# Kernel tuning notes

Hardware: AMD Instinct MI355X
Metric: run time of the kernel (lower is better)

The kernel has to match this reference:

```python
import jax, jax.numpy as jnp
import numpy as np
from jax import lax

B, N = 8, 107136          # batch, anchors (248*216*2)
SCORE_THRESH = 0.05
PRE_MAX = 2048            # nms_pre_max_sizes[0]
POST_MAX = 128            # nms_post_max_sizes[0]
IOU_THRESH = 0.5
NUM_DIR_BINS = 2
DIR_OFFSET = 0.0
POST_CENTER_RANGE = np.array([0.0, -39.68, -5.0, 69.12, 39.68, 5.0], np.float32)


def setup_inputs() -> dict:
    key = jax.random.key(0)
    k1, k2, k3, k4, k5 = jax.random.split(key, 5)
    box_preds = jax.random.normal(k1, (B, N, 7), jnp.float32) * 0.3
    cls_preds = jax.random.normal(k2, (B, N, 2), jnp.float32) * 2.0
    dir_preds = jax.random.normal(k3, (B, N, 2), jnp.float32)
    # realistic KITTI car anchors: (x, y, z, w, l, h, r)
    xs = jax.random.uniform(k4, (B, N), jnp.float32, 0.0, 69.12)
    ys = jax.random.uniform(k5, (B, N), jnp.float32, -39.68, 39.68)
    zs = jnp.full((B, N), -1.0, jnp.float32)
    w = jnp.full((B, N), 1.6, jnp.float32)
    l = jnp.full((B, N), 3.9, jnp.float32)
    h = jnp.full((B, N), 1.56, jnp.float32)
    r = jnp.broadcast_to(jnp.where(jnp.arange(N) % 2 == 0, 0.0, np.pi / 2).astype(jnp.float32), (B, N))
    anchors = jnp.stack([xs, ys, zs, w, l, h, r], axis=-1)
    return {"box_preds": box_preds, "cls_preds": cls_preds, "dir_preds": dir_preds, "anchors": anchors}


def _decode(bp, an):
    # GroundBox3dCoder.decode_torch (second/pointpillars), code order (x,y,z,w,l,h,r)
    xa, ya, za, wa, la, ha, ra = [an[..., i] for i in range(7)]
    xt, yt, zt, wt, lt, ht, rt = [bp[..., i] for i in range(7)]
    za = za + ha * 0.5
    diag = jnp.sqrt(la * la + wa * wa)
    xg = xt * diag + xa
    yg = yt * diag + ya
    zg = zt * ha + za
    lg = jnp.exp(lt) * la
    wg = jnp.exp(wt) * wa
    hg = jnp.exp(ht) * ha
    rg = rt + ra
    zg = zg - hg * 0.5
    return jnp.stack([xg, yg, zg, wg, lg, hg, rg], axis=-1)


def _standup(boxes):
    # boxes: [K,7] decoded; rotated 2d rect -> axis-aligned standup box (x1,y1,x2,y2)
    x, y, w, l, r = boxes[:, 0], boxes[:, 1], boxes[:, 3], boxes[:, 4], boxes[:, 6]
    c, s = jnp.abs(jnp.cos(r)), jnp.abs(jnp.sin(r))
    hx = 0.5 * (w * c + l * s)
    hy = 0.5 * (w * s + l * c)
    return jnp.stack([x - hx, y - hy, x + hx, y + hy], axis=-1)


def _pairwise_iou(bb):
    # bb: [K,4] standup boxes
    x1, y1, x2, y2 = bb[:, 0], bb[:, 1], bb[:, 2], bb[:, 3]
    area = (x2 - x1) * (y2 - y1)
    ix = jnp.maximum(0.0, jnp.minimum(x2[:, None], x2[None, :]) - jnp.maximum(x1[:, None], x1[None, :]))
    iy = jnp.maximum(0.0, jnp.minimum(y2[:, None], y2[None, :]) - jnp.maximum(y1[:, None], y1[None, :]))
    inter = ix * iy
    return inter / jnp.maximum(area[:, None] + area[None, :] - inter, 1e-8)


def _greedy_nms(ious, valid):
    K = valid.shape[0]
    idxs = jnp.arange(K)
    def body(i, keep):
        sup = (ious[i] > IOU_THRESH) & (idxs > i) & keep[i]
        return keep & ~sup
    return lax.fori_loop(0, K, body, valid)


def _limit_period(val, offset, period):
    return val - jnp.floor(val / period + offset) * period


def _predict_one(boxes, scores, dir_labels):
    # boxes [N,7], scores [N], dir_labels [N] int32 (already sorted? no: raw)
    masked = jnp.where(scores >= SCORE_THRESH, scores, -jnp.inf)
    top_s, idx = lax.top_k(masked, PRE_MAX)           # sorted desc
    b = boxes[idx]                                    # [K,7]
    dl = dir_labels[idx]
    valid = jnp.isfinite(top_s)
    ious = _pairwise_iou(_standup(b))
    keep = _greedy_nms(lax.stop_gradient(ious), valid)
    kept = jnp.where(keep, top_s, -jnp.inf)
    sel_s, sel_i = lax.top_k(kept, POST_MAX)
    sel_b = b[sel_i]
    sel_dl = dl[sel_i].astype(sel_b.dtype)
    period = 2.0 * np.pi / NUM_DIR_BINS
    dir_rot = _limit_period(sel_b[:, 6] - DIR_OFFSET, 0.0, period)
    new_r = dir_rot + DIR_OFFSET + period * sel_dl
    sel_b = jnp.concatenate([sel_b[:, :6], new_r[:, None]], axis=-1)
    pcr = jnp.asarray(POST_CENTER_RANGE)
    in_range = jnp.all(sel_b[:, :3] >= pcr[:3], axis=1) & jnp.all(sel_b[:, :3] <= pcr[3:], axis=1)
    mask = jnp.isfinite(sel_s) & in_range
    out_s = jnp.where(mask, sel_s, 0.0)
    out_b = jnp.where(mask[:, None], sel_b, 0.0)
    labels = jnp.zeros((POST_MAX,), jnp.int32)  # single fg class -> label 0
    return out_b, out_s, labels, mask


def reference(box_preds, cls_preds, dir_preds, anchors):
    decoded = _decode(box_preds, anchors)                    # [B,N,7]
    scores = jax.nn.softmax(cls_preds, axis=-1)[..., 1]      # [B,N]
    dir_labels = jnp.argmax(dir_preds, axis=-1).astype(jnp.int32)
    return jax.vmap(_predict_one)(decoded, scores, dir_labels)
```

## Files before the change

kernel.cpp:

```cpp
#include <hip/hip_runtime.h>
#include <stdint.h>

#define NB 8
#define NN 107136
#define TOTAL (NB * NN)
#define NPAIR (NN / 2)
#define PRE 2048
#define POST 128
#define CAP 4096
#define HBINS 128
#define KEYBASE 0xBF00u
#define SCORE_TH 0.05f
#define SH_BPB 53

static constexpr size_t OFF_SCORES = 0;
static constexpr size_t SZ_SCORES  = (size_t)TOTAL * 4;
static constexpr size_t OFF_HIST   = OFF_SCORES + SZ_SCORES;
static constexpr size_t SZ_HIST    = (size_t)NB * SH_BPB * HBINS * 4;
static constexpr size_t OFF_CNT    = OFF_HIST + SZ_HIST;
static constexpr size_t SZ_CNT     = (size_t)NB * 64 * 4;
static constexpr size_t OFF_CAND   = OFF_CNT + SZ_CNT + 256;
static constexpr size_t SZ_CAND    = (size_t)NB * CAP * 8;
static constexpr size_t OFF_SELS   = OFF_CAND + SZ_CAND;
static constexpr size_t OFF_SELI   = OFF_SELS + (size_t)NB * PRE * 4;
static constexpr size_t OFF_SELB   = OFF_SELI + (size_t)NB * PRE * 4;
static constexpr size_t OFF_SBB    = OFF_SELB + (size_t)NB * PRE * 7 * 4;
static constexpr size_t OFF_SAR    = OFF_SBB + (size_t)NB * PRE * 4 * 4;
static constexpr size_t OFF_MASK   = OFF_SAR + (size_t)NB * PRE * 4;
static constexpr size_t SZ_MASK    = (size_t)NB * PRE * 32 * 8;


__global__ void __launch_bounds__(256) k_scoreshist(const float* __restrict__ cls,
                                                    float* __restrict__ scores,
                                                    uint32_t* __restrict__ hp,
                                                    uint32_t* __restrict__ counts,
                                                    uint64_t* __restrict__ cand) {
    int b = blockIdx.y;
    int t = threadIdx.x;
    if (blockIdx.x == 0 && t == 0) counts[(size_t)b * 64] = 0u;
    if (blockIdx.x < 16)
        cand[(size_t)b * CAP + blockIdx.x * 256 + t] = 0ull;
    __shared__ uint32_t lh[HBINS];
    if (t < HBINS) lh[t] = 0u;
    __syncthreads();
    const float4* cp = (const float4*)cls + (size_t)b * NPAIR;
    float2* sp = (float2*)scores + (size_t)b * NPAIR;
#pragma unroll
    for (int k = 0; k < 4; k++) {
        int p = blockIdx.x * 1024 + k * 256 + t;
        if (p < NPAIR) {
            float4 c = cp[p];
            float m0 = fmaxf(c.x, c.y);
            float s0 = __fdiv_rn(expf(__fsub_rn(c.y, m0)),
                                 __fadd_rn(expf(__fsub_rn(c.x, m0)), expf(__fsub_rn(c.y, m0))));
            float m1 = fmaxf(c.z, c.w);
            float s1 = __fdiv_rn(expf(__fsub_rn(c.w, m1)),
                                 __fadd_rn(expf(__fsub_rn(c.z, m1)), expf(__fsub_rn(c.w, m1))));
            sp[p] = make_float2(s0, s1);
            if (s0 >= 0.5f) {
                uint32_t bin = ((__float_as_uint(s0) >> 16) | 0x8000u) - KEYBASE;
                if (bin > 127u) bin = 127u;
                atomicAdd(&lh[bin], 1u);
            }
            if (s1 >= 0.5f) {
                uint32_t bin = ((__float_as_uint(s1) >> 16) | 0x8000u) - KEYBASE;
                if (bin > 127u) bin = 127u;
                atomicAdd(&lh[bin], 1u);
            }
        }
    }
    __syncthreads();
    if (t < HBINS) hp[((size_t)b * SH_BPB + blockIdx.x) * HBINS + t] = lh[t];
}

__global__ void __launch_bounds__(256) k_compact(const float* __restrict__ scores,
                                                 const uint32_t* __restrict__ hp,
                                                 uint32_t* __restrict__ counts,
                                                 uint64_t* __restrict__ cand) {
    int g2 = blockIdx.x * 256 + threadIdx.x;
    int lane = threadIdx.x & 63, wid = threadIdx.x >> 6;
    int e0 = 2 * g2;
    int b = e0 / NN;

    uint32_t h0 = 0, h1 = 0;
    const uint32_t* hb = hp + (size_t)b * SH_BPB * HBINS;
#pragma unroll 4
    for (int sg = 0; sg < SH_BPB; sg++) {
        h0 += hb[sg * HBINS + 2 * lane];
        h1 += hb[sg * HBINS + 2 * lane + 1];
    }
    uint32_t v = h0 + h1;
    for (int off = 1; off < 64; off <<= 1) {
        uint32_t u = __shfl_down(v, off);
        if (lane + off >= 64) u = 0u;
        v += u;
    }
    uint32_t total = __shfl(v, 0);
    int c = -1;
    if (v - h0 >= PRE) c = 2 * lane + 1;
    else if (v >= PRE) c = 2 * lane;
    for (int off = 32; off > 0; off >>= 1) c = max(c, __shfl_xor(c, off));
    uint32_t Tb = (total >= PRE && c >= 0) ? (KEYBASE + (uint32_t)c) : 0u;

    float2 sv = ((const float2*)scores)[g2];
    uint32_t key0 = __float_as_uint(sv.x) | 0x80000000u;
    uint32_t key1 = __float_as_uint(sv.y) | 0x80000000u;
    bool p0 = (sv.x >= SCORE_TH) && ((key0 >> 16) >= Tb);
    bool p1 = (sv.y >= SCORE_TH) && ((key1 >> 16) >= Tb);
    uint64_t bal0 = __ballot(p0), bal1 = __ballot(p1);
    uint32_t n0 = (uint32_t)__popcll(bal0);
    uint32_t wcnt = n0 + (uint32_t)__popcll(bal1);
    uint64_t below = (1ull << lane) - 1ull;
    uint32_t off0 = (uint32_t)__popcll(bal0 & below);
    uint32_t off1 = n0 + (uint32_t)__popcll(bal1 & below);
    __shared__ uint32_t lcnt[2];
    __shared__ uint32_t gbase[2];
    __shared__ uint32_t wbase[4];
    int b0 = (blockIdx.x * 512) / NN;
    if (threadIdx.x < 2) lcnt[threadIdx.x] = 0u;
    __syncthreads();
    if (lane == 0 && wcnt) wbase[wid] = atomicAdd(&lcnt[b - b0], wcnt);
    __syncthreads();
    if (threadIdx.x < 2 && lcnt[threadIdx.x])
        gbase[threadIdx.x] = atomicAdd(&counts[(size_t)(b0 + threadIdx.x) * 64], lcnt[threadIdx.x]);
    __syncthreads();
    if (p0 | p1) {
        uint32_t base = gbase[b - b0] + wbase[wid];
        if (p0) {
            uint32_t slot = base + off0;
            if (slot < CAP)
                cand[(size_t)b * CAP + slot] =
                    ((uint64_t)key0 << 32) | (uint64_t)(0xFFFFFFFFu - (uint32_t)(e0 - b * NN));
        }
        if (p1) {
            uint32_t slot = base + off1;
            if (slot < CAP)
                cand[(size_t)b * CAP + slot] =
                    ((uint64_t)key1 << 32) | (uint64_t)(0xFFFFFFFFu - (uint32_t)(e0 + 1 - b * NN));
        }
    }
}

__global__ void __launch_bounds__(256) k_rank_decode(
        const uint64_t* __restrict__ cand, const uint32_t* __restrict__ counts,
        const float* __restrict__ box_preds, const float* __restrict__ anchors,
        float* __restrict__ selS, uint32_t* __restrict__ selI,
        float* __restrict__ selB, float* __restrict__ selBB, float* __restrict__ selA) {
    int b = blockIdx.y;
    int m = (int)counts[(size_t)b * 64]; if (m > CAP) m = CAP;
    int i0 = blockIdx.x * 256;
    if (i0 >= m) return;
    int t = threadIdx.x;
    int i = i0 + t;
    const uint64_t* cb = cand + (size_t)b * CAP;
    uint64_t mykey = (i < m) ? cb[i] : ~0ull;
    __shared__ uint64_t tile[512];
    uint32_t rank = 0;
    int ntiles = (m + 511) >> 9;
    for (int tt = 0; tt < ntiles; tt++) {
        int base = tt << 9;
        tile[t] = cb[base + t];
        tile[t + 256] = cb[base + 256 + t];
        __syncthreads();
#pragma unroll 16
        for (int j = 0; j < 512; j++)
            rank += (tile[j] > mykey) ? 1u : 0u;
        __syncthreads();
    }
    if (i >= m || rank >= PRE) return;

    size_t o = (size_t)b * PRE + rank;
    uint32_t key = (uint32_t)(mykey >> 32);
    uint32_t idx = 0xFFFFFFFFu - (uint32_t)(mykey & 0xFFFFFFFFull);
    float score = __uint_as_float(key & 0x7FFFFFFFu);
    const float* bp = box_preds + ((size_t)b * NN + idx) * 7;
    const float* an = anchors + ((size_t)b * NN + idx) * 7;
    float xa = an[0], ya = an[1], za = an[2], wa = an[3], la = an[4], ha = an[5], ra = an[6];
    float xt = bp[0], yt = bp[1], zt = bp[2], wt = bp[3], lt = bp[4], ht = bp[5], rt = bp[6];
    float za2  = __fadd_rn(za, __fmul_rn(ha, 0.5f));
    float diag = sqrtf(__fadd_rn(__fmul_rn(la, la), __fmul_rn(wa, wa)));
    float xg = __fadd_rn(__fmul_rn(xt, diag), xa);
    float yg = __fadd_rn(__fmul_rn(yt, diag), ya);
    float zg = __fadd_rn(__fmul_rn(zt, ha), za2);
    float lg = __fmul_rn(expf(lt), la);
    float wg = __fmul_rn(expf(wt), wa);
    float hg = __fmul_rn(expf(ht), ha);
    float rg = __fadd_rn(rt, ra);
    zg = __fsub_rn(zg, __fmul_rn(hg, 0.5f));
    selS[o] = score; selI[o] = idx;
    selB[o * 7 + 0] = xg; selB[o * 7 + 1] = yg; selB[o * 7 + 2] = zg;
    selB[o * 7 + 3] = wg; selB[o * 7 + 4] = lg; selB[o * 7 + 5] = hg;
    selB[o * 7 + 6] = rg;
    float cc = fabsf(cosf(rg)), ss = fabsf(sinf(rg));
    float hx = __fmul_rn(0.5f, __fadd_rn(__fmul_rn(wg, cc), __fmul_rn(lg, ss)));
    float hy = __fmul_rn(0.5f, __fadd_rn(__fmul_rn(wg, ss), __fmul_rn(lg, cc)));
    float x1 = __fsub_rn(xg, hx), y1 = __fsub_rn(yg, hy);
    float x2 = __fadd_rn(xg, hx), y2 = __fadd_rn(yg, hy);
    selBB[o * 4 + 0] = x1; selBB[o * 4 + 1] = y1;
    selBB[o * 4 + 2] = x2; selBB[o * 4 + 3] = y2;
    selA[o] = __fmul_rn(__fsub_rn(x2, x1), __fsub_rn(y2, y1));
}

__global__ void __launch_bounds__(256) k_iou(const float* __restrict__ selBB,
                                             const float* __restrict__ selA,
                                             uint64_t* __restrict__ maskrows) {
    int b = blockIdx.y;
    int r0 = blockIdx.x * 32;
    __shared__ float sx1[PRE], sy1[PRE], sx2[PRE], sy2[PRE], sar[PRE];
    int t = threadIdx.x;
    for (int i = t; i < PRE; i += 256) {
        const float* p = selBB + ((size_t)b * PRE + i) * 4;
        sx1[i] = p[0]; sy1[i] = p[1]; sx2[i] = p[2]; sy2[i] = p[3];
        sar[i] = selA[(size_t)b * PRE + i];
    }
    __syncthreads();
    int w  = t & 31;
    int rl = t >> 5;
    int jbase = w * 64;
    float rx1[4], ry1[4], rx2[4], ry2[4], rar[4];
    int rows[4];
#pragma unroll
    for (int p = 0; p < 4; p++) {
        int i = r0 + rl * 4 + p;
        rows[p] = i;
        rx1[p] = sx1[i]; ry1[p] = sy1[i]; rx2[p] = sx2[i]; ry2[p] = sy2[i]; rar[p] = sar[i];
    }
    uint64_t bits[4] = {0, 0, 0, 0};
    for (int jj = 0; jj < 64; jj++) {
        int j = jbase + ((jj + w) & 63);
        float xj1 = sx1[j], yj1 = sy1[j], xj2 = sx2[j], yj2 = sy2[j], aj = sar[j];
#pragma unroll
        for (int p = 0; p < 4; p++) {
            float ix = fmaxf(0.f, __fsub_rn(fminf(rx2[p], xj2), fmaxf(rx1[p], xj1)));
            float iy = fmaxf(0.f, __fsub_rn(fminf(ry2[p], yj2), fmaxf(ry1[p], yj1)));
            float inter = __fmul_rn(ix, iy);
            float den = fmaxf(__fsub_rn(__fadd_rn(rar[p], aj), inter), 1e-8f);
            if (inter > __fmul_rn(0.5f, den) && j > rows[p])
                bits[p] |= (1ull << (j - jbase));
        }
    }
#pragma unroll
    for (int p = 0; p < 4; p++)
        maskrows[((size_t)b * PRE + rows[p]) * 32 + w] = bits[p];
}

__global__ void __launch_bounds__(128) k_nms_final(
        const uint64_t* __restrict__ maskrows, const float* __restrict__ selS,
        const uint32_t* __restrict__ selI, const float* __restrict__ selB,
        const uint32_t* __restrict__ counts, const float* __restrict__ dir_preds,
        float* __restrict__ out) {
    int b = blockIdx.x;
    __shared__ int keptIdx[POST];
    __shared__ int keptCount;
    int t = threadIdx.x;
    int Mv = (int)counts[(size_t)b * 64]; if (Mv > PRE) Mv = PRE;
    if (t < 64) {
        uint64_t removed = 0ull;
        int kc = 0;
        const uint64_t* mb = maskrows + (size_t)b * PRE * 32;
        uint64_t pre[8];
#pragma unroll
        for (int d = 0; d < 8; d++)
            pre[d] = (t < 32 && d < Mv) ? mb[(size_t)d * 32 + t] : 0ull;
        for (int i = 0; i < Mv && kc < POST; i++) {
            uint64_t mrow = pre[i & 7];
            int nf = i + 8;
            pre[i & 7] = (t < 32 && nf < Mv) ? mb[(size_t)nf * 32 + t] : 0ull;
            uint64_t rw = __shfl(removed, i >> 6);
            if (!((rw >> (i & 63)) & 1ull)) {
                if (t == 0) keptIdx[kc] = i;
                kc++;
                removed |= mrow;
            }
        }
        if (t == 0) keptCount = kc;
    }
    __syncthreads();
    int kc = keptCount;
    size_t ob = (size_t)b * POST + t;
    float box[7] = {0.f, 0.f, 0.f, 0.f, 0.f, 0.f, 0.f};
    float sc = 0.f, mk = 0.f;
    if (t < kc) {
        int i = keptIdx[t];
        size_t o = (size_t)b * PRE + i;
        float s = selS[o];
        uint32_t idx = selI[o];
        const float* bx = selB + o * 7;
        float d0 = dir_preds[((size_t)b * NN + idx) * 2 + 0];
        float d1 = dir_preds[((size_t)b * NN + idx) * 2 + 1];
        float label = (d1 > d0) ? 1.0f : 0.0f;
        const float period = 3.14159265358979323846f;
        float r = bx[6];
        float dir_rot = __fsub_rn(r, __fmul_rn(floorf(__fdiv_rn(r, period)), period));
        float nr = __fadd_rn(dir_rot, __fmul_rn(period, label));
        float x = bx[0], y = bx[1], z = bx[2];
        bool in_range = (x >= 0.0f) && (y >= -39.68f) && (z >= -5.0f) &&
                        (x <= 69.12f) && (y <= 39.68f) && (z <= 5.0f);
        if (in_range) {
            box[0] = x; box[1] = y; box[2] = z;
            box[3] = bx[3]; box[4] = bx[4]; box[5] = bx[5]; box[6] = nr;
            sc = s; mk = 1.f;
        }
    }
    float* out_b = out;
    float* out_s = out + 7168;
    float* out_l = out + 8192;
    float* out_m = out + 9216;
    for (int c = 0; c < 7; c++) out_b[ob * 7 + c] = box[c];
    out_s[ob] = sc;
    out_l[ob] = 0.f;
    out_m[ob] = mk;
}

extern "C" void kernel_launch(void* const* d_in, const int* in_sizes, int n_in,
                              void* d_out, int out_size, void* d_ws, size_t ws_size,
                              hipStream_t stream) {
    const float* box_preds = (const float*)d_in[0];
    const float* cls_preds = (const float*)d_in[1];
    const float* dir_preds = (const float*)d_in[2];
    const float* anchors   = (const float*)d_in[3];
    float* out = (float*)d_out;
    char* ws = (char*)d_ws;

    float*    scores = (float*)(ws + OFF_SCORES);
    uint32_t* hp     = (uint32_t*)(ws + OFF_HIST);
    uint32_t* counts = (uint32_t*)(ws + OFF_CNT);
    uint64_t* cand   = (uint64_t*)(ws + OFF_CAND);
    float*    selS   = (float*)(ws + OFF_SELS);
    uint32_t* selI   = (uint32_t*)(ws + OFF_SELI);
    float*    selB   = (float*)(ws + OFF_SELB);
    float*    selBB  = (float*)(ws + OFF_SBB);
    float*    selA   = (float*)(ws + OFF_SAR);
    uint64_t* maskrows = (uint64_t*)(ws + OFF_MASK);

    dim3 gSH(SH_BPB, NB);
    k_scoreshist<<<gSH, 256, 0, stream>>>(cls_preds, scores, hp, counts, cand);
    k_compact<<<TOTAL / 512, 256, 0, stream>>>(scores, hp, counts, cand);
    dim3 gRank(CAP / 256, NB);
    k_rank_decode<<<gRank, 256, 0, stream>>>(cand, counts, box_preds, anchors,
                                             selS, selI, selB, selBB, selA);
    dim3 gIou(PRE / 32, NB);
    k_iou<<<gIou, 256, 0, stream>>>(selBB, selA, maskrows);
    k_nms_final<<<NB, 128, 0, stream>>>(maskrows, selS, selI, selB, counts,
                                        dir_preds, out);
}
```

Measured before the change: 209.0 us.

## Replace full IoU mask matrix with on-the-fly greedy NMS against kept boxes

Removes the separate all-pairs IoU kernel and the bitmask matrix. Instead one 64-lane wave per batch walks candidates in score order and tests each one only against the boxes already kept, which are held in registers (two per lane, up to 128), using a ballot to decide suppression. This avoids computing and writing the 2048x2048 mask and saves a kernel launch. In exchange the whole NMS becomes a serial loop on a single wave per batch with IoU arithmetic on the critical path, and the early exit once 128 boxes are kept still depends on the input data.

```diff
diff --git a/kernel.cpp b/kernel.cpp
--- a/kernel.cpp
+++ b/kernel.cpp
@@ -26,8 +26,6 @@
 static constexpr size_t OFF_SELB   = OFF_SELI + (size_t)NB * PRE * 4;
 static constexpr size_t OFF_SBB    = OFF_SELB + (size_t)NB * PRE * 7 * 4;
 static constexpr size_t OFF_SAR    = OFF_SBB + (size_t)NB * PRE * 4 * 4;
-static constexpr size_t OFF_MASK   = OFF_SAR + (size_t)NB * PRE * 4;
-static constexpr size_t SZ_MASK    = (size_t)NB * PRE * 32 * 8;
 
 
 __global__ void __launch_bounds__(256) k_scoreshist(const float* __restrict__ cls,
@@ -201,82 +199,57 @@
     selA[o] = __fmul_rn(__fsub_rn(x2, x1), __fsub_rn(y2, y1));
 }
 
-__global__ void __launch_bounds__(256) k_iou(const float* __restrict__ selBB,
-                                             const float* __restrict__ selA,
-                                             uint64_t* __restrict__ maskrows) {
-    int b = blockIdx.y;
-    int r0 = blockIdx.x * 32;
-    __shared__ float sx1[PRE], sy1[PRE], sx2[PRE], sy2[PRE], sar[PRE];
+__global__ void __launch_bounds__(128) k_nms(
+        const float* __restrict__ selBB, const float* __restrict__ selA,
+        const float* __restrict__ selS, const uint32_t* __restrict__ selI,
+        const float* __restrict__ selB, const uint32_t* __restrict__ counts,
+        const float* __restrict__ dir_preds, float* __restrict__ out) {
+    int b = blockIdx.x;
     int t = threadIdx.x;
-    for (int i = t; i < PRE; i += 256) {
-        const float* p = selBB + ((size_t)b * PRE + i) * 4;
-        sx1[i] = p[0]; sy1[i] = p[1]; sx2[i] = p[2]; sy2[i] = p[3];
-        sar[i] = selA[(size_t)b * PRE + i];
-    }
-    __syncthreads();
-    int w  = t & 31;
-    int rl = t >> 5;
-    int jbase = w * 64;
-    float rx1[4], ry1[4], rx2[4], ry2[4], rar[4];
-    int rows[4];
-#pragma unroll
-    for (int p = 0; p < 4; p++) {
-        int i = r0 + rl * 4 + p;
-        rows[p] = i;
-        rx1[p] = sx1[i]; ry1[p] = sy1[i]; rx2[p] = sx2[i]; ry2[p] = sy2[i]; rar[p] = sar[i];
-    }
-    uint64_t bits[4] = {0, 0, 0, 0};
-    for (int jj = 0; jj < 64; jj++) {
-        int j = jbase + ((jj + w) & 63);
-        float xj1 = sx1[j], yj1 = sy1[j], xj2 = sx2[j], yj2 = sy2[j], aj = sar[j];
-#pragma unroll
-        for (int p = 0; p < 4; p++) {
-            float ix = fmaxf(0.f, __fsub_rn(fminf(rx2[p], xj2), fmaxf(rx1[p], xj1)));
-            float iy = fmaxf(0.f, __fsub_rn(fminf(ry2[p], yj2), fmaxf(ry1[p], yj1)));
+    __shared__ float4 sbb[PRE];
+    __shared__ float  sar[PRE];
+    __shared__ int keptIdx[POST];
+    __shared__ int keptCountSh;
+    int Mv = (int)counts[(size_t)b * 64]; if (Mv > PRE) Mv = PRE;
+    const float4* bb4 = (const float4*)selBB + (size_t)b * PRE;
+    const float*  ar  = selA + (size_t)b * PRE;
+    for (int i = t; i < PRE; i += 128) {
+        sbb[i] = bb4[i];
+        sar[i] = ar[i];
+    }
+    __syncthreads();
+    if (t < 64) {
+        int lane = t;
+        float ax1 = 1e30f, ay1 = 1e30f, ax2 = 1e30f, ay2 = 1e30f, aar = 0.f;
+        float bx1 = 1e30f, by1 = 1e30f, bx2 = 1e30f, by2 = 1e30f, bar = 0.f;
+        int kc = 0;
+        for (int i = 0; i < Mv && kc < POST; i++) {
+            float4 c = sbb[i];
+            float ca = sar[i];
+            float ix = fmaxf(0.f, __fsub_rn(fminf(ax2, c.z), fmaxf(ax1, c.x)));
+            float iy = fmaxf(0.f, __fsub_rn(fminf(ay2, c.w), fmaxf(ay1, c.y)));
             float inter = __fmul_rn(ix, iy);
-            float den = fmaxf(__fsub_rn(__fadd_rn(rar[p], aj), inter), 1e-8f);
-            if (inter > __fmul_rn(0.5f, den) && j > rows[p])
-                bits[p] |= (1ull << (j - jbase));
-        }
-    }
-#pragma unroll
-    for (int p = 0; p < 4; p++)
-        maskrows[((size_t)b * PRE + rows[p]) * 32 + w] = bits[p];
-}
-
-__global__ void __launch_bounds__(128) k_nms_final(
-        const uint64_t* __restrict__ maskrows, const float* __restrict__ selS,
-        const uint32_t* __restrict__ selI, const float* __restrict__ selB,
-        const uint32_t* __restrict__ counts, const float* __restrict__ dir_preds,
-        float* __restrict__ out) {
-    int b = blockIdx.x;
-    __shared__ int keptIdx[POST];
-    __shared__ int keptCount;
-    int t = threadIdx.x;
-    int Mv = (int)counts[(size_t)b * 64]; if (Mv > PRE) Mv = PRE;
-    if (t < 64) {
-        uint64_t removed = 0ull;
-        int kc = 0;
-        const uint64_t* mb = maskrows + (size_t)b * PRE * 32;
-        uint64_t pre[8];
-#pragma unroll
-        for (int d = 0; d < 8; d++)
-            pre[d] = (t < 32 && d < Mv) ? mb[(size_t)d * 32 + t] : 0ull;
-        for (int i = 0; i < Mv && kc < POST; i++) {
-            uint64_t mrow = pre[i & 7];
-            int nf = i + 8;
-            pre[i & 7] = (t < 32 && nf < Mv) ? mb[(size_t)nf * 32 + t] : 0ull;
-            uint64_t rw = __shfl(removed, i >> 6);
-            if (!((rw >> (i & 63)) & 1ull)) {
-                if (t == 0) keptIdx[kc] = i;
+            float den = fmaxf(__fsub_rn(__fadd_rn(aar, ca), inter), 1e-8f);
+            bool sup = inter > __fmul_rn(0.5f, den);
+            ix = fmaxf(0.f, __fsub_rn(fminf(bx2, c.z), fmaxf(bx1, c.x)));
+            iy = fmaxf(0.f, __fsub_rn(fminf(by2, c.w), fmaxf(by1, c.y)));
+            inter = __fmul_rn(ix, iy);
+            den = fmaxf(__fsub_rn(__fadd_rn(bar, ca), inter), 1e-8f);
+            sup = sup || (inter > __fmul_rn(0.5f, den));
+            if (__ballot(sup) == 0ull) {
+                if (lane == 0) keptIdx[kc] = i;
+                if (kc < 64) {
+                    if (lane == kc) { ax1 = c.x; ay1 = c.y; ax2 = c.z; ay2 = c.w; aar = ca; }
+                } else {
+                    if (lane == kc - 64) { bx1 = c.x; by1 = c.y; bx2 = c.z; by2 = c.w; bar = ca; }
+                }
                 kc++;
-                removed |= mrow;
             }
         }
-        if (t == 0) keptCount = kc;
-    }
-    __syncthreads();
-    int kc = keptCount;
+        if (lane == 0) keptCountSh = kc;
+    }
+    __syncthreads();
+    int kc = keptCountSh;
     size_t ob = (size_t)b * POST + t;
     float box[7] = {0.f, 0.f, 0.f, 0.f, 0.f, 0.f, 0.f};
     float sc = 0.f, mk = 0.f;
@@ -331,7 +304,6 @@
     float*    selB   = (float*)(ws + OFF_SELB);
     float*    selBB  = (float*)(ws + OFF_SBB);
     float*    selA   = (float*)(ws + OFF_SAR);
-    uint64_t* maskrows = (uint64_t*)(ws + OFF_MASK);
 
     dim3 gSH(SH_BPB, NB);
     k_scoreshist<<<gSH, 256, 0, stream>>>(cls_preds, scores, hp, counts, cand);
@@ -339,8 +311,6 @@
     dim3 gRank(CAP / 256, NB);
     k_rank_decode<<<gRank, 256, 0, stream>>>(cand, counts, box_preds, anchors,
                                              selS, selI, selB, selBB, selA);
-    dim3 gIou(PRE / 32, NB);
-    k_iou<<<gIou, 256, 0, stream>>>(selBB, selA, maskrows);
-    k_nms_final<<<NB, 128, 0, stream>>>(maskrows, selS, selI, selB, counts,
-                                        dir_preds, out);
-}
+    k_nms<<<NB, 128, 0, stream>>>(selBB, selA, selS, selI, selB, counts,
+                                  dir_preds, out);
+}
```

Result: faster. 178.0 us (-14.8%).
